# Optimization experiments

Measured on AMD Instinct MI355X. Metric: run time of the kernel, lower is better.

The kernel has to match this reference:

```python
import jax, jax.numpy as jnp
import numpy as np

N_CLASSES = 91  # classes 0..90; class 0 (background) is excluded from the mean


def setup_inputs() -> dict:
    key = jax.random.key(0)
    k1, k2 = jax.random.split(key)
    B, H, W = 64, 512, 512
    # label maps with integer class ids in [0, 91); `inputs` stored as float32
    # to mirror the original (compared elementwise against integer i)
    inputs = jax.random.randint(k1, (B, H, W), 0, N_CLASSES).astype(jnp.float32)
    targets = jax.random.randint(k2, (B, H, W), 0, N_CLASSES).astype(jnp.int32)
    return {"inputs": inputs, "targets": targets, "smooth": 1}


def reference(inputs, targets, smooth):
    # Single-pass histogram formulation of the original per-class loop:
    #   intersection_i = #{p : inputs[p]==i and targets[p]==i}
    #   total_i        = #{inputs==i} + #{targets==i}
    #   union_i        = total_i - intersection_i
    n = N_CLASSES
    inp = inputs.reshape(-1).astype(jnp.int32)
    tgt = targets.reshape(-1).astype(jnp.int32)
    cnt_in = jnp.bincount(inp, length=n).astype(jnp.float32)
    cnt_tg = jnp.bincount(tgt, length=n).astype(jnp.float32)
    # positions where prediction == target contribute to that class's intersection;
    # mismatches are routed to a dummy bin n and dropped
    inter = jnp.bincount(jnp.where(inp == tgt, inp, n), length=n + 1)[:n].astype(jnp.float32)
    union = cnt_in + cnt_tg - inter
    smooth_f = jnp.float32(smooth)
    iou = (inter[1:] + smooth_f) / (union[1:] + smooth_f)  # classes 1..n-1
    return jnp.sum(iou) / (n - 1)
```

## Files before the change

kernel.cpp:

```cpp
#include <hip/hip_runtime.h>

#define NCLS 91
#define NP (NCLS * NCLS)
#define NPPAD 8320
#define NHIST (3 * NCLS)
#define BS 256
#define NWAVES 4
#define NT 16
#define CHUNK 64

typedef const __attribute__((address_space(1))) void* gas_t;
typedef __attribute__((address_space(3))) void* las_t;

__global__ __launch_bounds__(BS) void miou_hist(const float* __restrict__ inp,
                                                const int* __restrict__ tgt,
                                                unsigned int* __restrict__ ws) {
    __shared__ unsigned int ph[NPPAD];
    __shared__ float4 sbuf[NWAVES][2][2][CHUNK];

    uint4* z = (uint4*)ph;
    for (int i = threadIdx.x; i < NPPAD / 4; i += BS) z[i] = make_uint4(0u, 0u, 0u, 0u);
    __syncthreads();

    const int w = threadIdx.x >> 6;
    const int l = threadIdx.x & 63;
    const long base = ((long)blockIdx.x * NWAVES + w) * NT;
    const float4* in4 = (const float4*)inp;
    const int4*  tg4 = (const int4*)tgt;

    auto stage = [&](int slot, int it) {
        const float4* g0 = in4 + (base + it) * CHUNK + l;
        const int4*  g1 = tg4 + (base + it) * CHUNK + l;
        __builtin_amdgcn_global_load_lds((gas_t)g0, (las_t)&sbuf[w][slot][0][0], 16, 0, 0);
        __builtin_amdgcn_global_load_lds((gas_t)g1, (las_t)&sbuf[w][slot][1][0], 16, 0, 0);
    };

    auto process = [&](int slot) {
        float4 f = sbuf[w][slot][0][l];
        int4  t = *(const int4*)&sbuf[w][slot][1][l];
        int a0 = (int)f.x, a1 = (int)f.y, a2 = (int)f.z, a3 = (int)f.w;
        atomicAdd(&ph[a0 * NCLS + t.x], 1u);
        atomicAdd(&ph[a1 * NCLS + t.y], 1u);
        atomicAdd(&ph[a2 * NCLS + t.z], 1u);
        atomicAdd(&ph[a3 * NCLS + t.w], 1u);
    };

    stage(0, 0);
    stage(1, 1);
    #pragma unroll
    for (int it = 0; it < NT; ++it) {
        if (it < NT - 1) {
            asm volatile("s_waitcnt vmcnt(2)" ::: "memory");
        } else {
            asm volatile("s_waitcnt vmcnt(0)" ::: "memory");
        }
        __builtin_amdgcn_sched_barrier(0);
        process(it & 1);
        if (it + 2 < NT) stage(it & 1, it + 2);
    }
    __syncthreads();

    int t = threadIdx.x;
    if (t < NCLS) {
        const unsigned int* p = ph + t * NCLS;
        unsigned int s0 = 0, s1 = 0, s2 = 0, s3 = 0;
        int k = 0;
        for (; k + 3 < NCLS; k += 4) { s0 += p[k]; s1 += p[k+1]; s2 += p[k+2]; s3 += p[k+3]; }
        for (; k < NCLS; ++k) s0 += p[k];
        unsigned int s = s0 + s1 + s2 + s3;
        if (s) atomicAdd(&ws[t], s);
        unsigned int d = p[t];
        if (d) atomicAdd(&ws[2 * NCLS + t], d);
    } else if (t >= 128 && t < 128 + NCLS) {
        int c = t - 128;
        unsigned int s0 = 0, s1 = 0, s2 = 0, s3 = 0;
        int a = 0;
        for (; a + 3 < NCLS; a += 4) {
            s0 += ph[a * NCLS + c];
            s1 += ph[(a + 1) * NCLS + c];
            s2 += ph[(a + 2) * NCLS + c];
            s3 += ph[(a + 3) * NCLS + c];
        }
        for (; a < NCLS; ++a) s0 += ph[a * NCLS + c];
        unsigned int s = s0 + s1 + s2 + s3;
        if (s) atomicAdd(&ws[NCLS + c], s);
    }
}

__global__ void miou_tail(const float* __restrict__ inp, const int* __restrict__ tgt,
                          unsigned int* __restrict__ ws, int e0, int n) {
    int i = e0 + blockIdx.x * 256 + threadIdx.x;
    if (i < n) {
        int a = (int)inp[i];
        int t = tgt[i];
        atomicAdd(&ws[a], 1u);
        atomicAdd(&ws[NCLS + t], 1u);
        if (a == t) atomicAdd(&ws[2 * NCLS + a], 1u);
    }
}

__global__ void miou_finalize(const unsigned int* __restrict__ ws,
                              const int* __restrict__ smooth_p,
                              float* __restrict__ out) {
    int lane = threadIdx.x;
    float s = (float)(*smooth_p);
    float acc = 0.f;
    for (int c = 1 + lane; c < NCLS; c += 64) {
        float ci = (float)ws[c];
        float ct = (float)ws[NCLS + c];
        float it = (float)ws[2 * NCLS + c];
        float un = ci + ct - it;
        acc += (it + s) / (un + s);
    }
    #pragma unroll
    for (int off = 32; off; off >>= 1) acc += __shfl_down(acc, off);
    if (lane == 0) out[0] = acc / (float)(NCLS - 1);
}

extern "C" void kernel_launch(void* const* d_in, const int* in_sizes, int n_in,
                              void* d_out, int out_size, void* d_ws, size_t ws_size,
                              hipStream_t stream) {
    const float* inp = (const float*)d_in[0];
    const int* tgt = (const int*)d_in[1];
    const int* smooth_p = (const int*)d_in[2];
    float* out = (float*)d_out;
    unsigned int* ws = (unsigned int*)d_ws;

    int n = in_sizes[0];
    int n4 = n >> 2;
    int nblk = n4 / (NWAVES * NT * CHUNK);
    int e0 = nblk * NWAVES * NT * CHUNK * 4;

    hipMemsetAsync(ws, 0, NHIST * sizeof(unsigned int), stream);
    if (nblk > 0)
        miou_hist<<<nblk, BS, 0, stream>>>(inp, tgt, ws);
    if (e0 < n)
        miou_tail<<<(n - e0 + 255) / 256, 256, 0, stream>>>(inp, tgt, ws, e0, n);
    miou_finalize<<<1, 64, 0, stream>>>(ws, smooth_p, out);
}
```

Baseline: 169.4 us.

## Pack pair histogram into 16-bit LDS counters and deepen the async load pipeline

Shrinks the per-block LDS pair histogram by packing two 16-bit target-class counters into each 32-bit word; the reductions unpack them. The global-to-LDS prefetch grows from double buffering to a 6-deep ring, and each wave handles 32 tiles instead of 16. The aim is to hide load latency behind the LDS atomics. In exchange, the staging buffers take more LDS, which may lower occupancy. Neighbouring classes now share a word, which can add atomic contention. The wrapped prefetch indices also issue a few redundant tile loads at the end of the loop.

```diff
diff --git a/kernel.cpp b/kernel.cpp
--- a/kernel.cpp
+++ b/kernel.cpp
@@ -1,12 +1,14 @@
 #include <hip/hip_runtime.h>
 
 #define NCLS 91
-#define NP (NCLS * NCLS)
-#define NPPAD 8320
+#define NW 46
+#define NPW (NCLS * NW)
+#define NPPAD 4192
 #define NHIST (3 * NCLS)
 #define BS 256
 #define NWAVES 4
-#define NT 16
+#define NT 32
+#define D 6
 #define CHUNK 64
 
 typedef const __attribute__((address_space(1))) void* gas_t;
@@ -16,7 +18,7 @@
                                                 const int* __restrict__ tgt,
                                                 unsigned int* __restrict__ ws) {
     __shared__ unsigned int ph[NPPAD];
-    __shared__ float4 sbuf[NWAVES][2][2][CHUNK];
+    __shared__ float4 sbuf[NWAVES][D][2][CHUNK];
 
     uint4* z = (uint4*)ph;
     for (int i = threadIdx.x; i < NPPAD / 4; i += BS) z[i] = make_uint4(0u, 0u, 0u, 0u);
@@ -28,61 +30,50 @@
     const float4* in4 = (const float4*)inp;
     const int4*  tg4 = (const int4*)tgt;
 
-    auto stage = [&](int slot, int it) {
-        const float4* g0 = in4 + (base + it) * CHUNK + l;
-        const int4*  g1 = tg4 + (base + it) * CHUNK + l;
+    auto stage = [&](int slot, int tile) {
+        const float4* g0 = in4 + (base + tile) * CHUNK + l;
+        const int4*  g1 = tg4 + (base + tile) * CHUNK + l;
         __builtin_amdgcn_global_load_lds((gas_t)g0, (las_t)&sbuf[w][slot][0][0], 16, 0, 0);
         __builtin_amdgcn_global_load_lds((gas_t)g1, (las_t)&sbuf[w][slot][1][0], 16, 0, 0);
     };
 
-    auto process = [&](int slot) {
-        float4 f = sbuf[w][slot][0][l];
-        int4  t = *(const int4*)&sbuf[w][slot][1][l];
-        int a0 = (int)f.x, a1 = (int)f.y, a2 = (int)f.z, a3 = (int)f.w;
-        atomicAdd(&ph[a0 * NCLS + t.x], 1u);
-        atomicAdd(&ph[a1 * NCLS + t.y], 1u);
-        atomicAdd(&ph[a2 * NCLS + t.z], 1u);
-        atomicAdd(&ph[a3 * NCLS + t.w], 1u);
+    auto pin = [&](int a, int tv) {
+        atomicAdd(&ph[a * NW + (tv >> 1)], 1u << ((tv & 1) << 4));
     };
 
-    stage(0, 0);
-    stage(1, 1);
+    #pragma unroll
+    for (int p = 0; p < D - 1; ++p) stage(p, p);
+
     #pragma unroll
     for (int it = 0; it < NT; ++it) {
-        if (it < NT - 1) {
-            asm volatile("s_waitcnt vmcnt(2)" ::: "memory");
-        } else {
-            asm volatile("s_waitcnt vmcnt(0)" ::: "memory");
-        }
+        asm volatile("s_waitcnt vmcnt(%0)" :: "i"(2 * (D - 2)) : "memory");
         __builtin_amdgcn_sched_barrier(0);
-        process(it & 1);
-        if (it + 2 < NT) stage(it & 1, it + 2);
+        stage((it + D - 1) % D, (it + D - 1) % NT);
+        float4 f = sbuf[w][it % D][0][l];
+        int4  t = *(const int4*)&sbuf[w][it % D][1][l];
+        pin((int)f.x, t.x);
+        pin((int)f.y, t.y);
+        pin((int)f.z, t.z);
+        pin((int)f.w, t.w);
     }
     __syncthreads();
 
     int t = threadIdx.x;
     if (t < NCLS) {
-        const unsigned int* p = ph + t * NCLS;
-        unsigned int s0 = 0, s1 = 0, s2 = 0, s3 = 0;
-        int k = 0;
-        for (; k + 3 < NCLS; k += 4) { s0 += p[k]; s1 += p[k+1]; s2 += p[k+2]; s3 += p[k+3]; }
-        for (; k < NCLS; ++k) s0 += p[k];
-        unsigned int s = s0 + s1 + s2 + s3;
+        const unsigned int* p = ph + t * NW;
+        unsigned int s = 0;
+        #pragma unroll 2
+        for (int k = 0; k < NW; ++k) { unsigned int v = p[k]; s += (v & 0xFFFFu) + (v >> 16); }
         if (s) atomicAdd(&ws[t], s);
-        unsigned int d = p[t];
+        unsigned int dv = p[t >> 1];
+        unsigned int d = (t & 1) ? (dv >> 16) : (dv & 0xFFFFu);
         if (d) atomicAdd(&ws[2 * NCLS + t], d);
     } else if (t >= 128 && t < 128 + NCLS) {
         int c = t - 128;
-        unsigned int s0 = 0, s1 = 0, s2 = 0, s3 = 0;
-        int a = 0;
-        for (; a + 3 < NCLS; a += 4) {
-            s0 += ph[a * NCLS + c];
-            s1 += ph[(a + 1) * NCLS + c];
-            s2 += ph[(a + 2) * NCLS + c];
-            s3 += ph[(a + 3) * NCLS + c];
-        }
-        for (; a < NCLS; ++a) s0 += ph[a * NCLS + c];
-        unsigned int s = s0 + s1 + s2 + s3;
+        int sh = (c & 1) << 4;
+        unsigned int s = 0;
+        #pragma unroll 2
+        for (int a = 0; a < NCLS; ++a) s += (ph[a * NW + (c >> 1)] >> sh) & 0xFFFFu;
         if (s) atomicAdd(&ws[NCLS + c], s);
     }
 }
@@ -127,9 +118,9 @@
     unsigned int* ws = (unsigned int*)d_ws;
 
     int n = in_sizes[0];
-    int n4 = n >> 2;
-    int nblk = n4 / (NWAVES * NT * CHUNK);
-    int e0 = nblk * NWAVES * NT * CHUNK * 4;
+    int eper = BS * 4 * NT;
+    int nblk = n / eper;
+    int e0 = nblk * eper;
 
     hipMemsetAsync(ws, 0, NHIST * sizeof(unsigned int), stream);
     if (nblk > 0)
```

New measurement: 165.3 us. -2.4%, faster.

## Replace LDS-staged pipelined histogram with fixed-grid direct loads at 512 threads

Applied to the files above, without the earlier changes.

Drops the global_load_lds double-buffered staging and its manual waitcnt scheduling. Each thread now loads two float4/int4 pairs straight into registers and does the shared-memory pair-histogram atomics, over a fixed grid of 4096 blocks of 512 threads. Each block builds and reduces its own 91x91 histogram, so the grid size sets how many blocks pay the zero-fill, reduction and global-atomic overhead. The old explicit copy/compute overlap is lost. Occupancy now rests on larger blocks and hardware latency hiding, and a grid-stride fallback covers inputs of other sizes.

```diff
diff --git a/kernel.cpp b/kernel.cpp
--- a/kernel.cpp
+++ b/kernel.cpp
@@ -2,61 +2,47 @@
 
 #define NCLS 91
 #define NP (NCLS * NCLS)
-#define NPPAD 8320
+#define NPPAD 8284
 #define NHIST (3 * NCLS)
-#define BS 256
-#define NWAVES 4
-#define NT 16
-#define CHUNK 64
+#define BS 512
+#define NBLK 4096
 
-typedef const __attribute__((address_space(1))) void* gas_t;
-typedef __attribute__((address_space(3))) void* las_t;
-
-__global__ __launch_bounds__(BS) void miou_hist(const float* __restrict__ inp,
-                                                const int* __restrict__ tgt,
-                                                unsigned int* __restrict__ ws) {
+__global__ __launch_bounds__(BS, 8) void miou_hist(const float* __restrict__ inp,
+                                                   const int* __restrict__ tgt,
+                                                   unsigned int* __restrict__ ws,
+                                                   int n4) {
     __shared__ unsigned int ph[NPPAD];
-    __shared__ float4 sbuf[NWAVES][2][2][CHUNK];
-
     uint4* z = (uint4*)ph;
     for (int i = threadIdx.x; i < NPPAD / 4; i += BS) z[i] = make_uint4(0u, 0u, 0u, 0u);
     __syncthreads();
 
-    const int w = threadIdx.x >> 6;
-    const int l = threadIdx.x & 63;
-    const long base = ((long)blockIdx.x * NWAVES + w) * NT;
     const float4* in4 = (const float4*)inp;
-    const int4*  tg4 = (const int4*)tgt;
+    const int4* tg4 = (const int4*)tgt;
+    const int i0 = blockIdx.x * BS + threadIdx.x;
+    const int stride = NBLK * BS;
 
-    auto stage = [&](int slot, int it) {
-        const float4* g0 = in4 + (base + it) * CHUNK + l;
-        const int4*  g1 = tg4 + (base + it) * CHUNK + l;
-        __builtin_amdgcn_global_load_lds((gas_t)g0, (las_t)&sbuf[w][slot][0][0], 16, 0, 0);
-        __builtin_amdgcn_global_load_lds((gas_t)g1, (las_t)&sbuf[w][slot][1][0], 16, 0, 0);
-    };
-
-    auto process = [&](int slot) {
-        float4 f = sbuf[w][slot][0][l];
-        int4  t = *(const int4*)&sbuf[w][slot][1][l];
-        int a0 = (int)f.x, a1 = (int)f.y, a2 = (int)f.z, a3 = (int)f.w;
-        atomicAdd(&ph[a0 * NCLS + t.x], 1u);
-        atomicAdd(&ph[a1 * NCLS + t.y], 1u);
-        atomicAdd(&ph[a2 * NCLS + t.z], 1u);
-        atomicAdd(&ph[a3 * NCLS + t.w], 1u);
-    };
-
-    stage(0, 0);
-    stage(1, 1);
-    #pragma unroll
-    for (int it = 0; it < NT; ++it) {
-        if (it < NT - 1) {
-            asm volatile("s_waitcnt vmcnt(2)" ::: "memory");
-        } else {
-            asm volatile("s_waitcnt vmcnt(0)" ::: "memory");
+    if (i0 + stride < n4) {
+        float4 f0 = in4[i0];
+        int4  t0 = tg4[i0];
+        float4 f1 = in4[i0 + stride];
+        int4  t1 = tg4[i0 + stride];
+        atomicAdd(&ph[(int)f0.x * NCLS + t0.x], 1u);
+        atomicAdd(&ph[(int)f0.y * NCLS + t0.y], 1u);
+        atomicAdd(&ph[(int)f0.z * NCLS + t0.z], 1u);
+        atomicAdd(&ph[(int)f0.w * NCLS + t0.w], 1u);
+        atomicAdd(&ph[(int)f1.x * NCLS + t1.x], 1u);
+        atomicAdd(&ph[(int)f1.y * NCLS + t1.y], 1u);
+        atomicAdd(&ph[(int)f1.z * NCLS + t1.z], 1u);
+        atomicAdd(&ph[(int)f1.w * NCLS + t1.w], 1u);
+    } else {
+        for (int i = i0; i < n4; i += stride) {
+            float4 f = in4[i];
+            int4 t = tg4[i];
+            atomicAdd(&ph[(int)f.x * NCLS + t.x], 1u);
+            atomicAdd(&ph[(int)f.y * NCLS + t.y], 1u);
+            atomicAdd(&ph[(int)f.z * NCLS + t.z], 1u);
+            atomicAdd(&ph[(int)f.w * NCLS + t.w], 1u);
         }
-        __builtin_amdgcn_sched_barrier(0);
-        process(it & 1);
-        if (it + 2 < NT) stage(it & 1, it + 2);
     }
     __syncthreads();
 
@@ -128,12 +114,10 @@
 
     int n = in_sizes[0];
     int n4 = n >> 2;
-    int nblk = n4 / (NWAVES * NT * CHUNK);
-    int e0 = nblk * NWAVES * NT * CHUNK * 4;
+    int e0 = (n4 & ~3) * 0 + (n & ~3);
 
     hipMemsetAsync(ws, 0, NHIST * sizeof(unsigned int), stream);
-    if (nblk > 0)
-        miou_hist<<<nblk, BS, 0, stream>>>(inp, tgt, ws);
+    miou_hist<<<NBLK, BS, 0, stream>>>(inp, tgt, ws, n4);
     if (e0 < n)
         miou_tail<<<(n - e0 + 255) / 256, 256, 0, stream>>>(inp, tgt, ws, e0, n);
     miou_finalize<<<1, 64, 0, stream>>>(ws, smooth_p, out);
```

New measurement: 235.5 us. 1.39x slower.
